# Kernel optimization log

Hardware: AMD Instinct MI355X
Metric: run time of the kernel (lower is better)

Reference implementation:

```python
import jax, jax.numpy as jnp
import numpy as np

B1, B2, N, D = 1, 128, 256, 256
H, C = 8, 32
OUT = 256


def setup_inputs() -> dict:
    key = jax.random.key(0)
    ks = jax.random.split(key, 8)
    in_data = jax.random.normal(ks[0], (B1, B2, N, D), dtype=jnp.float32)
    # binary mask, mostly unmasked
    mask = (jax.random.uniform(ks[1], (B1, B2, N)) > 0.1).astype(jnp.float32)
    nonbatched_bias = jax.random.normal(ks[2], (B1, H, N, N), dtype=jnp.float32)
    scale = 1.0 / np.sqrt(D)
    w_qkv = jax.random.normal(ks[3], (3 * H * C, D), dtype=jnp.float32) * scale  # torch Linear [out,in]
    w_gate = jax.random.normal(ks[4], (H * C, D), dtype=jnp.float32) * scale
    gating_bias = jnp.ones((H * C,), dtype=jnp.float32)
    w_o = jax.random.normal(ks[5], (OUT, H * C), dtype=jnp.float32) * scale
    b_o = jnp.zeros((OUT,), dtype=jnp.float32)
    return {
        "in_data": in_data,
        "mask": mask,
        "nonbatched_bias": nonbatched_bias,
        "w_qkv": w_qkv,
        "w_gate": w_gate,
        "gating_bias": gating_bias,
        "w_o": w_o,
        "b_o": b_o,
    }


def reference(in_data, mask, nonbatched_bias, w_qkv, w_gate, gating_bias, w_o, b_o):
    scaling = C ** (-0.5)
    # fused QKV projection (no bias): [b1,b2,n, 3*h*c]
    qkv = jnp.einsum("xynd,ed->xyne", in_data, w_qkv)
    q, k, v = jnp.split(qkv, 3, axis=-1)

    def heads(t):  # [b1,b2,n,h*c] -> [b1,b2,h,n,c]
        return t.reshape(B1, B2, N, H, C).transpose(0, 1, 3, 2, 4)

    q, k, v = heads(q) * scaling, heads(k), heads(v)
    logits = jnp.einsum("xyhqc,xyhkc->xyhqk", q, k)
    mask_bias = (1e9 * (mask - 1.0))[:, :, None, None, :]  # [b1,b2,1,1,n]
    logits = logits + mask_bias + nonbatched_bias[:, None]  # [b1,b2,h,q,k]
    weights = jax.nn.softmax(logits, axis=-1)
    wa = jnp.einsum("xyhqk,xyhkc->xyhqc", weights, v)
    wa = wa.transpose(0, 1, 3, 2, 4).reshape(B1, B2, N, H * C)
    # sigmoid gating: sigmoid(gate_linear(x) + gating_bias) * weighted_avg
    gate = jax.nn.sigmoid(jnp.einsum("xynd,ed->xyne", in_data, w_gate) + gating_bias)
    wa = gate * wa
    out = jnp.einsum("xyne,oe->xyno", wa, w_o) + b_o
    return out
```

## Files before the change

### kernel.cpp

```cpp
#include <hip/hip_runtime.h>
#include <stdint.h>

#define B2 128
#define NSEQ 256
#define DIM 256
#define NH 8
#define CH 32

typedef __attribute__((ext_vector_type(8))) __bf16 bf16x8;
typedef __attribute__((ext_vector_type(8))) unsigned short u16x8;
typedef __attribute__((ext_vector_type(4))) unsigned short u16x4;
typedef __attribute__((ext_vector_type(4))) float f32x4;

__device__ __forceinline__ unsigned short f2bf(float f) {
  unsigned int u = __builtin_bit_cast(unsigned int, f);
  u += 0x7FFFu + ((u >> 16) & 1u);
  return (unsigned short)(u >> 16);
}
__device__ __forceinline__ float bf2f(unsigned short h) {
  unsigned int u = ((unsigned int)h) << 16;
  return __builtin_bit_cast(float, u);
}
__device__ __forceinline__ bf16x8 as_bf(u16x8 v) { return __builtin_bit_cast(bf16x8, v); }

__device__ __forceinline__ void gload16(void* lds, const void* g) {
  __builtin_amdgcn_global_load_lds(
      (__attribute__((address_space(1))) void*)(g),
      (__attribute__((address_space(3))) void*)(lds), 16, 0, 0);
}

__global__ void k_convert(const float* __restrict__ x, const float* __restrict__ wqkv,
                          const float* __restrict__ wgate, const float* __restrict__ wo,
                          unsigned short* __restrict__ xb, unsigned short* __restrict__ wallb,
                          unsigned short* __restrict__ wob) {
  const int NX = 8388608, NWALL = 262144, NWO = 65536;
  int i = blockIdx.x * blockDim.x + threadIdx.x;
  int total4 = (NX + NWALL + NWO) >> 2;
  if (i >= total4) return;
  int e = i << 2;
  float4 v;
  unsigned short* dst;
  if (e < NX) {
    v = *reinterpret_cast<const float4*>(x + e);
    dst = xb + e;
  } else if (e < NX + NWALL) {
    int o = e - NX;
    v = (o < 196608) ? *reinterpret_cast<const float4*>(wqkv + o)
                     : *reinterpret_cast<const float4*>(wgate + (o - 196608));
    dst = wallb + o;
  } else {
    int o = e - NX - NWALL;
    v = *reinterpret_cast<const float4*>(wo + o);
    dst = wob + o;
  }
  u16x4 r;
  r[0] = f2bf(v.x); r[1] = f2bf(v.y); r[2] = f2bf(v.z); r[3] = f2bf(v.w);
  *reinterpret_cast<u16x4*>(dst) = r;
}

template <int MODE>
__launch_bounds__(256, 2)
__global__ void k_gemm(const unsigned short* __restrict__ A, const unsigned short* __restrict__ Bw,
                       unsigned short* __restrict__ qs, unsigned short* __restrict__ ksb,
                       unsigned short* __restrict__ vsb, unsigned short* __restrict__ gateb,
                       const float* __restrict__ gbias,
                       float* __restrict__ outp, const float* __restrict__ bo) {
  __shared__ __attribute__((aligned(16))) unsigned short As[2][8192];
  __shared__ __attribute__((aligned(16))) unsigned short Bs[2][8192];
  const int tid = threadIdx.x, lane = tid & 63, w = tid >> 6;
  const int wr = w >> 1, wc = w & 1;
  const int m0 = blockIdx.x * 128, n0 = blockIdx.y * 128;

  auto stage = [&](unsigned short* sbuf, const unsigned short* gsrc, int row0, int k0) {
#pragma unroll
    for (int q2 = 0; q2 < 4; ++q2) {
      int ob = (w * 4 + q2) * 1024 + (lane << 4);
      int r = ob >> 7, cb = ob & 127;
      int scb = cb ^ ((r & 7) << 4);
      const unsigned short* g = gsrc + (size_t)(row0 + r) * 256 + k0 + (scb >> 1);
      gload16(sbuf + (size_t)(w * 4 + q2) * 512, g);
    }
  };

  f32x4 acc[4][4];
#pragma unroll
  for (int i = 0; i < 4; ++i) {
#pragma unroll
    for (int j = 0; j < 4; ++j) acc[i][j] = (f32x4){0.f, 0.f, 0.f, 0.f};
  }

  stage(As[0], A, m0, 0);
  stage(Bs[0], Bw, n0, 0);
  asm volatile("s_waitcnt vmcnt(0)" ::: "memory");
  __syncthreads();

#pragma unroll
  for (int kt = 0; kt < 4; ++kt) {
    const int cur = kt & 1;
    if (kt < 3) {
      stage(As[cur ^ 1], A, m0, (kt + 1) * 64);
      stage(Bs[cur ^ 1], Bw, n0, (kt + 1) * 64);
    }
#pragma unroll
    for (int kk = 0; kk < 2; ++kk) {
      bf16x8 af[4], bfv[4];
      const int cb = kk * 64 + ((lane >> 4) << 4);
#pragma unroll
      for (int fr = 0; fr < 4; ++fr) {
        int ra = wr * 64 + fr * 16 + (lane & 15);
        int off = ra * 128 + (cb ^ ((ra & 7) << 4));
        af[fr] = *reinterpret_cast<const bf16x8*>((const char*)As[cur] + off);
      }
#pragma unroll
      for (int fc = 0; fc < 4; ++fc) {
        int rb = wc * 64 + fc * 16 + (lane & 15);
        int off = rb * 128 + (cb ^ ((rb & 7) << 4));
        bfv[fc] = *reinterpret_cast<const bf16x8*>((const char*)Bs[cur] + off);
      }
#pragma unroll
      for (int fr = 0; fr < 4; ++fr) {
#pragma unroll
        for (int fc = 0; fc < 4; ++fc)
          acc[fr][fc] = __builtin_amdgcn_mfma_f32_16x16x32_bf16(af[fr], bfv[fc], acc[fr][fc], 0, 0, 0);
      }
    }
    asm volatile("s_waitcnt vmcnt(0)" ::: "memory");
    __syncthreads();
  }

  if (MODE == 0) {
#pragma unroll
    for (int fr = 0; fr < 4; ++fr) {
      int mrow = m0 + wr * 64 + fr * 16 + ((lane >> 4) << 2);
      int b = mrow >> 8, n = mrow & 255;
#pragma unroll
      for (int fc = 0; fc < 4; ++fc) {
        int e = n0 + wc * 64 + fc * 16 + (lane & 15);
        int which = e >> 8, loc = e & 255, hh = loc >> 5, cc = loc & 31;
#pragma unroll
        for (int i = 0; i < 4; ++i) {
          float v = acc[fr][fc][i];
          size_t idx = ((size_t)(b * 8 + hh) * 256 + (n + i)) * 32 + cc;
          if (which == 0) {
            qs[idx] = f2bf(v * 0.17677669529663687f);
          } else if (which == 1) {
            ksb[idx] = f2bf(v);
          } else if (which == 2) {
            vsb[idx] = f2bf(v);
          } else {
            float gsig = 1.0f / (1.0f + __expf(-(v + gbias[loc])));
            gateb[idx] = f2bf(gsig);
          }
        }
      }
    }
  } else {
#pragma unroll
    for (int fr = 0; fr < 4; ++fr) {
      int mrow = m0 + wr * 64 + fr * 16 + ((lane >> 4) << 2);
#pragma unroll
      for (int fc = 0; fc < 4; ++fc) {
        int e = n0 + wc * 64 + fc * 16 + (lane & 15);
        float bb = bo[e];
#pragma unroll
        for (int i = 0; i < 4; ++i)
          outp[(size_t)(mrow + i) * 256 + e] = acc[fr][fc][i] + bb;
      }
    }
  }
}

__launch_bounds__(256, 3)
__global__ void k_attn(const unsigned short* __restrict__ qs, const unsigned short* __restrict__ ksb,
                       const unsigned short* __restrict__ vsb, const unsigned short* __restrict__ gateb,
                       const float* __restrict__ mask, const float* __restrict__ nb,
                       unsigned short* __restrict__ wag) {
  __shared__ __attribute__((aligned(16))) unsigned short vt[32][264];
  __shared__ __attribute__((aligned(16))) unsigned short pch[4][2][16][72];
  __shared__ __attribute__((aligned(16))) float mb[256];
  __shared__ float invl[4][16];
  const int tid = threadIdx.x, lane = tid & 63, w = tid >> 6;
  const int l15 = lane & 15, hi = lane >> 4;
  const int b = blockIdx.x, h = blockIdx.y;
  const size_t bh = (size_t)(b * 8 + h);
  const unsigned short* kbase = ksb + bh * 8192;
  const unsigned short* vbase = vsb + bh * 8192;
  const unsigned short* qbase = qs + bh * 8192;
  const float* nbh = nb + (size_t)h * 65536;

  mb[tid] = 1e9f * (mask[b * 256 + tid] - 1.0f);
  {
    const unsigned short* vrow = vbase + tid * 32;
#pragma unroll
    for (int c0 = 0; c0 < 32; c0 += 8) {
      u16x8 vv = *reinterpret_cast<const u16x8*>(vrow + c0);
#pragma unroll
      for (int j = 0; j < 8; ++j) vt[c0 + j][tid] = vv[j];
    }
  }
  u16x8 kf[16];
#pragma unroll
  for (int kt = 0; kt < 16; ++kt)
    kf[kt] = *reinterpret_cast<const u16x8*>(kbase + (kt * 16 + l15) * 32 + hi * 8);
  __syncthreads();

  const f32x4 zero = {0.f, 0.f, 0.f, 0.f};
#pragma unroll 1
  for (int fr = 0; fr < 4; ++fr) {
    const int q0 = w * 64 + fr * 16;
    u16x8 qf = *reinterpret_cast<const u16x8*>(qbase + (q0 + l15) * 32 + hi * 8);
    f32x4 sacc[16];
    __builtin_amdgcn_s_setprio(1);
#pragma unroll
    for (int kt = 0; kt < 16; ++kt)
      sacc[kt] = __builtin_amdgcn_mfma_f32_16x16x32_bf16(as_bf(kf[kt]), as_bf(qf), zero, 0, 0, 0);
    __builtin_amdgcn_s_setprio(0);

    const float* nbq = nbh + (size_t)(q0 + l15) * 256;
#pragma unroll
    for (int kt = 0; kt < 16; ++kt) {
      float4 nb4 = *reinterpret_cast<const float4*>(nbq + kt * 16 + hi * 4);
      float4 mb4 = *reinterpret_cast<const float4*>(&mb[kt * 16 + hi * 4]);
      sacc[kt][0] += mb4.x + nb4.x;
      sacc[kt][1] += mb4.y + nb4.y;
      sacc[kt][2] += mb4.z + nb4.z;
      sacc[kt][3] += mb4.w + nb4.w;
    }
    float mx = -3.0e38f;
#pragma unroll
    for (int kt = 0; kt < 16; ++kt) {
#pragma unroll
      for (int i = 0; i < 4; ++i) mx = fmaxf(mx, sacc[kt][i]);
    }
    mx = fmaxf(mx, __shfl_xor(mx, 16));
    mx = fmaxf(mx, __shfl_xor(mx, 32));

    float sum = 0.f;
    f32x4 wacc[2];
    wacc[0] = zero; wacc[1] = zero;
#pragma unroll
    for (int c = 0; c < 4; ++c) {
      const int buf = c & 1;
#pragma unroll
      for (int ktl = 0; ktl < 4; ++ktl) {
        const int kt = c * 4 + ktl;
        u16x4 pv;
#pragma unroll
        for (int i = 0; i < 4; ++i) {
          float p = __expf(sacc[kt][i] - mx);
          sum += p;
          pv[i] = f2bf(p);
        }
        *reinterpret_cast<u16x4*>(&pch[w][buf][l15][ktl * 16 + hi * 4]) = pv;
      }
      asm volatile("s_waitcnt lgkmcnt(0)" ::: "memory");
      __builtin_amdgcn_sched_barrier(0);
      __builtin_amdgcn_s_setprio(1);
#pragma unroll
      for (int ks2 = 0; ks2 < 2; ++ks2) {
        bf16x8 pa = *reinterpret_cast<const bf16x8*>(&pch[w][buf][l15][ks2 * 32 + hi * 8]);
#pragma unroll
        for (int ct = 0; ct < 2; ++ct) {
          bf16x8 vb = *reinterpret_cast<const bf16x8*>(&vt[ct * 16 + l15][c * 64 + ks2 * 32 + hi * 8]);
          wacc[ct] = __builtin_amdgcn_mfma_f32_16x16x32_bf16(pa, vb, wacc[ct], 0, 0, 0);
        }
      }
      __builtin_amdgcn_s_setprio(0);
    }
    sum += __shfl_xor(sum, 16);
    sum += __shfl_xor(sum, 32);
    const float inv = 1.0f / sum;
    if (hi == 0) invl[w][l15] = inv;

    float* et = reinterpret_cast<float*>(&pch[w][0][0][0]);
#pragma unroll
    for (int ct = 0; ct < 2; ++ct) {
#pragma unroll
      for (int i = 0; i < 4; ++i)
        et[(hi * 4 + i) * 36 + ct * 16 + l15] = wacc[ct][i];
    }
    asm volatile("s_waitcnt lgkmcnt(0)" ::: "memory");
    __builtin_amdgcn_sched_barrier(0);
    const int eq = lane >> 2, eh = lane & 3;
    float4 v0 = *reinterpret_cast<const float4*>(&et[eq * 36 + eh * 8]);
    float4 v1 = *reinterpret_cast<const float4*>(&et[eq * 36 + eh * 8 + 4]);
    const float iv = invl[w][eq];
    const int qrow = q0 + eq;
    u16x8 g = *reinterpret_cast<const u16x8*>(gateb + bh * 8192 + qrow * 32 + eh * 8);
    u16x8 ov;
    ov[0] = f2bf(bf2f(g[0]) * v0.x * iv);
    ov[1] = f2bf(bf2f(g[1]) * v0.y * iv);
    ov[2] = f2bf(bf2f(g[2]) * v0.z * iv);
    ov[3] = f2bf(bf2f(g[3]) * v0.w * iv);
    ov[4] = f2bf(bf2f(g[4]) * v1.x * iv);
    ov[5] = f2bf(bf2f(g[5]) * v1.y * iv);
    ov[6] = f2bf(bf2f(g[6]) * v1.z * iv);
    ov[7] = f2bf(bf2f(g[7]) * v1.w * iv);
    *reinterpret_cast<u16x8*>(wag + ((size_t)(b * 256 + qrow)) * 256 + h * 32 + eh * 8) = ov;
    asm volatile("s_waitcnt lgkmcnt(0)" ::: "memory");
    __builtin_amdgcn_sched_barrier(0);
  }
}

extern "C" void kernel_launch(void* const* d_in, const int* in_sizes, int n_in,
                              void* d_out, int out_size, void* d_ws, size_t ws_size,
                              hipStream_t stream) {
  const float* x     = (const float*)d_in[0];
  const float* mask  = (const float*)d_in[1];
  const float* nb    = (const float*)d_in[2];
  const float* wqkv  = (const float*)d_in[3];
  const float* wgate = (const float*)d_in[4];
  const float* gbias = (const float*)d_in[5];
  const float* wo    = (const float*)d_in[6];
  const float* bo    = (const float*)d_in[7];
  float* outp = (float*)d_out;

  char* ws = (char*)d_ws;
  unsigned short* xb    = (unsigned short*)(ws);
  unsigned short* wallb = (unsigned short*)(ws + 16777216);
  unsigned short* wob   = (unsigned short*)(ws + 17301504);
  unsigned short* qs    = (unsigned short*)(ws + 17432576);
  unsigned short* ksb   = (unsigned short*)(ws + 34209792);
  unsigned short* vsb   = (unsigned short*)(ws + 50987008);
  unsigned short* gateb = (unsigned short*)(ws + 67764224);
  unsigned short* wag   = xb;

  k_convert<<<dim3(8512), dim3(256), 0, stream>>>(x, wqkv, wgate, wo, xb, wallb, wob);
  k_gemm<0><<<dim3(256, 8), dim3(256), 0, stream>>>(xb, wallb, qs, ksb, vsb, gateb, gbias, nullptr, nullptr);
  k_attn<<<dim3(128, 8), dim3(256), 0, stream>>>(qs, ksb, vsb, gateb, mask, nb, wag);
  k_gemm<1><<<dim3(256, 2), dim3(256), 0, stream>>>(wag, wob, nullptr, nullptr, nullptr, nullptr, nullptr, outp, bo);
}
```

Before: 139.7 us.

## Restructure attention P@V via register shuffles and swizzle GEMM block order

The attention kernel now keeps softmax probabilities in registers, packing them with v_cvt_pk_bf16_f32 and redistributing them across lanes with shuffles. This replaces the per-wave LDS staging and its waitcnt barriers. K moves from registers into padded LDS, V^T gets an XOR-swizzled layout, and the bias and gate loads are prefetched and split into halves. The gating epilogue writes directly from the MFMA accumulator layout, giving scattered 2-byte stores instead of 16-byte vector stores. Both GEMM launches switch to a 1D grid with a grouped tile order for better L2 reuse.

After: 211.7 us. 51.5% more time.

```diff
diff --git a/kernel.cpp b/kernel.cpp
--- a/kernel.cpp
+++ b/kernel.cpp
@@ -10,6 +10,7 @@
 typedef __attribute__((ext_vector_type(8))) __bf16 bf16x8;
 typedef __attribute__((ext_vector_type(8))) unsigned short u16x8;
 typedef __attribute__((ext_vector_type(4))) unsigned short u16x4;
+typedef __attribute__((ext_vector_type(4))) unsigned int u32x4;
 typedef __attribute__((ext_vector_type(4))) float f32x4;
 
 __device__ __forceinline__ unsigned short f2bf(float f) {
@@ -22,6 +23,11 @@
   return __builtin_bit_cast(float, u);
 }
 __device__ __forceinline__ bf16x8 as_bf(u16x8 v) { return __builtin_bit_cast(bf16x8, v); }
+__device__ __forceinline__ unsigned int cvtpk(float lo, float hi) {
+  unsigned int r;
+  asm("v_cvt_pk_bf16_f32 %0, %1, %2" : "=v"(r) : "v"(lo), "v"(hi));
+  return r;
+}
 
 __device__ __forceinline__ void gload16(void* lds, const void* g) {
   __builtin_amdgcn_global_load_lds(
@@ -69,7 +75,10 @@
   __shared__ __attribute__((aligned(16))) unsigned short Bs[2][8192];
   const int tid = threadIdx.x, lane = tid & 63, w = tid >> 6;
   const int wr = w >> 1, wc = w & 1;
-  const int m0 = blockIdx.x * 128, n0 = blockIdx.y * 128;
+  const int bid = blockIdx.x;
+  int m0, n0;
+  if (MODE == 0) { m0 = ((bid & 7) + ((bid >> 6) << 3)) * 128; n0 = ((bid >> 3) & 7) * 128; }
+  else           { m0 = ((bid & 7) + ((bid >> 4) << 3)) * 128; n0 = ((bid >> 3) & 1) * 128; }
 
   auto stage = [&](unsigned short* sbuf, const unsigned short* gsrc, int row0, int k0) {
 #pragma unroll
@@ -175,10 +184,9 @@
                        const unsigned short* __restrict__ vsb, const unsigned short* __restrict__ gateb,
                        const float* __restrict__ mask, const float* __restrict__ nb,
                        unsigned short* __restrict__ wag) {
-  __shared__ __attribute__((aligned(16))) unsigned short vt[32][264];
-  __shared__ __attribute__((aligned(16))) unsigned short pch[4][2][16][72];
+  __shared__ __attribute__((aligned(16))) unsigned short Kl[256 * 40];
+  __shared__ __attribute__((aligned(16))) unsigned short vt[32 * 256];
   __shared__ __attribute__((aligned(16))) float mb[256];
-  __shared__ float invl[4][16];
   const int tid = threadIdx.x, lane = tid & 63, w = tid >> 6;
   const int l15 = lane & 15, hi = lane >> 4;
   const int b = blockIdx.x, h = blockIdx.y;
@@ -186,6 +194,7 @@
   const unsigned short* kbase = ksb + bh * 8192;
   const unsigned short* vbase = vsb + bh * 8192;
   const unsigned short* qbase = qs + bh * 8192;
+  const unsigned short* gbase = gateb + bh * 8192;
   const float* nbh = nb + (size_t)h * 65536;
 
   mb[tid] = 1e9f * (mask[b * 256 + tid] - 1.0f);
@@ -195,37 +204,76 @@
     for (int c0 = 0; c0 < 32; c0 += 8) {
       u16x8 vv = *reinterpret_cast<const u16x8*>(vrow + c0);
 #pragma unroll
-      for (int j = 0; j < 8; ++j) vt[c0 + j][tid] = vv[j];
-    }
-  }
-  u16x8 kf[16];
-#pragma unroll
-  for (int kt = 0; kt < 16; ++kt)
-    kf[kt] = *reinterpret_cast<const u16x8*>(kbase + (kt * 16 + l15) * 32 + hi * 8);
+      for (int j = 0; j < 8; ++j) {
+        int c = c0 + j;
+        vt[c * 256 + (((tid * 2) ^ ((c & 15) << 4)) >> 1)] = vv[j];
+      }
+    }
+    const unsigned short* krow = kbase + tid * 32;
+#pragma unroll
+    for (int c8 = 0; c8 < 4; ++c8)
+      *reinterpret_cast<u16x8*>(&Kl[tid * 40 + c8 * 8]) =
+          *reinterpret_cast<const u16x8*>(krow + c8 * 8);
+  }
   __syncthreads();
 
   const f32x4 zero = {0.f, 0.f, 0.f, 0.f};
+  const int srcA = l15 + (((2 * hi) & 3) << 4);
+  const int srcB = l15 + (((2 * hi + 1) & 3) << 4);
+  const bool gsel = (hi >= 2);
+
 #pragma unroll 1
   for (int fr = 0; fr < 4; ++fr) {
     const int q0 = w * 64 + fr * 16;
+    const float* nbq = nbh + (size_t)(q0 + l15) * 256;
+
+    f32x4 nbv0[8];
+#pragma unroll
+    for (int kt = 0; kt < 8; ++kt) {
+      float4 t = *reinterpret_cast<const float4*>(nbq + kt * 16 + hi * 4);
+      nbv0[kt] = (f32x4){t.x, t.y, t.z, t.w};
+    }
+    unsigned short gpre[8];
+#pragma unroll
+    for (int ct = 0; ct < 2; ++ct)
+#pragma unroll
+      for (int i = 0; i < 4; ++i)
+        gpre[ct * 4 + i] = gbase[(q0 + hi * 4 + i) * 32 + ct * 16 + l15];
     u16x8 qf = *reinterpret_cast<const u16x8*>(qbase + (q0 + l15) * 32 + hi * 8);
+
     f32x4 sacc[16];
     __builtin_amdgcn_s_setprio(1);
 #pragma unroll
-    for (int kt = 0; kt < 16; ++kt)
-      sacc[kt] = __builtin_amdgcn_mfma_f32_16x16x32_bf16(as_bf(kf[kt]), as_bf(qf), zero, 0, 0, 0);
+    for (int kt = 0; kt < 16; ++kt) {
+      bf16x8 kf = *reinterpret_cast<const bf16x8*>(
+          (const char*)Kl + (kt * 16 + l15) * 80 + hi * 16);
+      sacc[kt] = __builtin_amdgcn_mfma_f32_16x16x32_bf16(kf, as_bf(qf), zero, 0, 0, 0);
+    }
     __builtin_amdgcn_s_setprio(0);
 
-    const float* nbq = nbh + (size_t)(q0 + l15) * 256;
-#pragma unroll
-    for (int kt = 0; kt < 16; ++kt) {
-      float4 nb4 = *reinterpret_cast<const float4*>(nbq + kt * 16 + hi * 4);
+#pragma unroll
+    for (int kt = 0; kt < 8; ++kt) {
       float4 mb4 = *reinterpret_cast<const float4*>(&mb[kt * 16 + hi * 4]);
-      sacc[kt][0] += mb4.x + nb4.x;
-      sacc[kt][1] += mb4.y + nb4.y;
-      sacc[kt][2] += mb4.z + nb4.z;
-      sacc[kt][3] += mb4.w + nb4.w;
-    }
+      sacc[kt][0] += mb4.x + nbv0[kt][0];
+      sacc[kt][1] += mb4.y + nbv0[kt][1];
+      sacc[kt][2] += mb4.z + nbv0[kt][2];
+      sacc[kt][3] += mb4.w + nbv0[kt][3];
+    }
+    f32x4 nbv1[8];
+#pragma unroll
+    for (int kt = 0; kt < 8; ++kt) {
+      float4 t = *reinterpret_cast<const float4*>(nbq + (kt + 8) * 16 + hi * 4);
+      nbv1[kt] = (f32x4){t.x, t.y, t.z, t.w};
+    }
+#pragma unroll
+    for (int kt = 0; kt < 8; ++kt) {
+      float4 mb4 = *reinterpret_cast<const float4*>(&mb[(kt + 8) * 16 + hi * 4]);
+      sacc[kt + 8][0] += mb4.x + nbv1[kt][0];
+      sacc[kt + 8][1] += mb4.y + nbv1[kt][1];
+      sacc[kt + 8][2] += mb4.z + nbv1[kt][2];
+      sacc[kt + 8][3] += mb4.w + nbv1[kt][3];
+    }
+
     float mx = -3.0e38f;
 #pragma unroll
     for (int kt = 0; kt < 16; ++kt) {
@@ -236,69 +284,62 @@
     mx = fmaxf(mx, __shfl_xor(mx, 32));
 
     float sum = 0.f;
-    f32x4 wacc[2];
-    wacc[0] = zero; wacc[1] = zero;
-#pragma unroll
-    for (int c = 0; c < 4; ++c) {
-      const int buf = c & 1;
-#pragma unroll
-      for (int ktl = 0; ktl < 4; ++ktl) {
-        const int kt = c * 4 + ktl;
-        u16x4 pv;
-#pragma unroll
-        for (int i = 0; i < 4; ++i) {
-          float p = __expf(sacc[kt][i] - mx);
-          sum += p;
-          pv[i] = f2bf(p);
-        }
-        *reinterpret_cast<u16x4*>(&pch[w][buf][l15][ktl * 16 + hi * 4]) = pv;
-      }
-      asm volatile("s_waitcnt lgkmcnt(0)" ::: "memory");
-      __builtin_amdgcn_sched_barrier(0);
-      __builtin_amdgcn_s_setprio(1);
-#pragma unroll
-      for (int ks2 = 0; ks2 < 2; ++ks2) {
-        bf16x8 pa = *reinterpret_cast<const bf16x8*>(&pch[w][buf][l15][ks2 * 32 + hi * 8]);
-#pragma unroll
-        for (int ct = 0; ct < 2; ++ct) {
-          bf16x8 vb = *reinterpret_cast<const bf16x8*>(&vt[ct * 16 + l15][c * 64 + ks2 * 32 + hi * 8]);
-          wacc[ct] = __builtin_amdgcn_mfma_f32_16x16x32_bf16(pa, vb, wacc[ct], 0, 0, 0);
-        }
-      }
-      __builtin_amdgcn_s_setprio(0);
+    unsigned int pk0[16], pk1[16];
+#pragma unroll
+    for (int kt = 0; kt < 16; ++kt) {
+      float p0 = __expf(sacc[kt][0] - mx);
+      float p1 = __expf(sacc[kt][1] - mx);
+      float p2 = __expf(sacc[kt][2] - mx);
+      float p3 = __expf(sacc[kt][3] - mx);
+      sum += (p0 + p1) + (p2 + p3);
+      pk0[kt] = cvtpk(p0, p1);
+      pk1[kt] = cvtpk(p2, p3);
     }
     sum += __shfl_xor(sum, 16);
     sum += __shfl_xor(sum, 32);
     const float inv = 1.0f / sum;
-    if (hi == 0) invl[w][l15] = inv;
-
-    float* et = reinterpret_cast<float*>(&pch[w][0][0][0]);
+
+    f32x4 wacc[2];
+    wacc[0] = zero; wacc[1] = zero;
+    __builtin_amdgcn_s_setprio(1);
+#pragma unroll
+    for (int ks2 = 0; ks2 < 8; ++ks2) {
+      unsigned int a0A = (unsigned int)__shfl((int)pk0[2 * ks2], srcA);
+      unsigned int a1A = (unsigned int)__shfl((int)pk1[2 * ks2], srcA);
+      unsigned int a2A = (unsigned int)__shfl((int)pk0[2 * ks2], srcB);
+      unsigned int a3A = (unsigned int)__shfl((int)pk1[2 * ks2], srcB);
+      unsigned int a0B = (unsigned int)__shfl((int)pk0[2 * ks2 + 1], srcA);
+      unsigned int a1B = (unsigned int)__shfl((int)pk1[2 * ks2 + 1], srcA);
+      unsigned int a2B = (unsigned int)__shfl((int)pk0[2 * ks2 + 1], srcB);
+      unsigned int a3B = (unsigned int)__shfl((int)pk1[2 * ks2 + 1], srcB);
+      u32x4 afu;
+      afu[0] = gsel ? a0B : a0A;
+      afu[1] = gsel ? a1B : a1A;
+      afu[2] = gsel ? a2B : a2A;
+      afu[3] = gsel ? a3B : a3A;
+      bf16x8 af = __builtin_bit_cast(bf16x8, afu);
+#pragma unroll
+      for (int ct = 0; ct < 2; ++ct) {
+        bf16x8 vb = *reinterpret_cast<const bf16x8*>(
+            (const char*)vt + (ct * 16 + l15) * 512 + ((ks2 * 64 + hi * 16) ^ (l15 << 4)));
+        wacc[ct] = __builtin_amdgcn_mfma_f32_16x16x32_bf16(af, vb, wacc[ct], 0, 0, 0);
+      }
+    }
+    __builtin_amdgcn_s_setprio(0);
+
+    float iv[4];
+#pragma unroll
+    for (int i = 0; i < 4; ++i)
+      iv[i] = __shfl(inv, hi * 4 + i);
 #pragma unroll
     for (int ct = 0; ct < 2; ++ct) {
 #pragma unroll
-      for (int i = 0; i < 4; ++i)
-        et[(hi * 4 + i) * 36 + ct * 16 + l15] = wacc[ct][i];
-    }
-    asm volatile("s_waitcnt lgkmcnt(0)" ::: "memory");
-    __builtin_amdgcn_sched_barrier(0);
-    const int eq = lane >> 2, eh = lane & 3;
-    float4 v0 = *reinterpret_cast<const float4*>(&et[eq * 36 + eh * 8]);
-    float4 v1 = *reinterpret_cast<const float4*>(&et[eq * 36 + eh * 8 + 4]);
-    const float iv = invl[w][eq];
-    const int qrow = q0 + eq;
-    u16x8 g = *reinterpret_cast<const u16x8*>(gateb + bh * 8192 + qrow * 32 + eh * 8);
-    u16x8 ov;
-    ov[0] = f2bf(bf2f(g[0]) * v0.x * iv);
-    ov[1] = f2bf(bf2f(g[1]) * v0.y * iv);
-    ov[2] = f2bf(bf2f(g[2]) * v0.z * iv);
-    ov[3] = f2bf(bf2f(g[3]) * v0.w * iv);
-    ov[4] = f2bf(bf2f(g[4]) * v1.x * iv);
-    ov[5] = f2bf(bf2f(g[5]) * v1.y * iv);
-    ov[6] = f2bf(bf2f(g[6]) * v1.z * iv);
-    ov[7] = f2bf(bf2f(g[7]) * v1.w * iv);
-    *reinterpret_cast<u16x8*>(wag + ((size_t)(b * 256 + qrow)) * 256 + h * 32 + eh * 8) = ov;
-    asm volatile("s_waitcnt lgkmcnt(0)" ::: "memory");
-    __builtin_amdgcn_sched_barrier(0);
+      for (int i = 0; i < 4; ++i) {
+        int q = q0 + hi * 4 + i;
+        float o = bf2f(gpre[ct * 4 + i]) * wacc[ct][i] * iv[i];
+        wag[((size_t)(b * 256 + q)) * 256 + h * 32 + ct * 16 + l15] = f2bf(o);
+      }
+    }
   }
 }
 
@@ -326,7 +367,7 @@
   unsigned short* wag   = xb;
 
   k_convert<<<dim3(8512), dim3(256), 0, stream>>>(x, wqkv, wgate, wo, xb, wallb, wob);
-  k_gemm<0><<<dim3(256, 8), dim3(256), 0, stream>>>(xb, wallb, qs, ksb, vsb, gateb, gbias, nullptr, nullptr);
+  k_gemm<0><<<dim3(2048), dim3(256), 0, stream>>>(xb, wallb, qs, ksb, vsb, gateb, gbias, nullptr, nullptr);
   k_attn<<<dim3(128, 8), dim3(256), 0, stream>>>(qs, ksb, vsb, gateb, mask, nb, wag);
-  k_gemm<1><<<dim3(256, 2), dim3(256), 0, stream>>>(wag, wob, nullptr, nullptr, nullptr, nullptr, nullptr, outp, bo);
-}
+  k_gemm<1><<<dim3(512), dim3(256), 0, stream>>>(wag, wob, nullptr, nullptr, nullptr, nullptr, nullptr, outp, bo);
+}
```
